# Kernel tuning notes

Measured on AMD Instinct MI355X. Metric: run time of the kernel, lower is better.

## Reference

```python
import jax, jax.numpy as jnp
import numpy as np

LEVEL = 3  # J
B3_TAPS = (1.0 / 16, 1.0 / 4, 3.0 / 8, 1.0 / 4, 1.0 / 16)  # h1, fixed non-trainable


def _b3_conv2d(x, d):
    """Separable 5-tap B3-spline conv with dilation d and reflect padding.

    Equivalent to torch Conv2d(1,1,5,dilation=d,padding=2*d,padding_mode='reflect')
    with weight = outer(h1, h1): the dense 5x5 kernel is separable.
    x: (B, H, W) -> (B, H, W)
    """
    w = [jnp.asarray(t, x.dtype) for t in B3_TAPS]
    pad = 2 * d  # effective half-width of dilated 5-tap kernel
    H, W = x.shape[1], x.shape[2]
    # conv along H
    xp = jnp.pad(x, ((0, 0), (pad, pad), (0, 0)), mode='reflect')
    x = sum(w[k] * xp[:, k * d:k * d + H, :] for k in range(5))
    # conv along W
    xp = jnp.pad(x, ((0, 0), (0, 0), (pad, pad)), mode='reflect')
    x = sum(w[k] * xp[:, :, k * d:k * d + W] for k in range(5))
    return x


def setup_inputs() -> dict:
    key = jax.random.key(0)
    x = jax.random.normal(key, (8, 1024, 1024), dtype=jnp.float32)
    return {"x": x}


def reference(x) -> jnp.ndarray:
    # c_j = h_j * c_{j-1};  w_j = c_{j-1} - c_j;  return [w_1..w_J, c_J] stacked on axis 1
    outs = []
    c = x
    for j in range(LEVEL):
        c_next = _b3_conv2d(c, 2 ** j)
        outs.append(c - c_next)
        c = c_next
    outs.append(c)
    return jnp.stack(outs, axis=1)  # (B, J+1, H, W)
```

## Files before the change

### kernel.cpp

```cpp
#include <hip/hip_runtime.h>

#define DEVINL __device__ __forceinline__


constexpr int W_IMG = 1024;
constexpr int H_IMG = 1024;
constexpr int TX = 32;
constexpr int TY = 32;
constexpr int HALO = 16;
constexpr int SW = 68;
constexpr int GXT = W_IMG / TX;
constexpr int GYT = H_IMG / TY;
constexpr int SHA = 60;
constexpr int SHB = 56;

constexpr float TP0 = 1.0f / 16.0f;
constexpr float TP1 = 1.0f / 4.0f;
constexpr float TP2 = 3.0f / 8.0f;

typedef float f32x4 __attribute__((ext_vector_type(4)));

template <int CTRL>
DEVINL float dppf(float x) {
    return __int_as_float(__builtin_amdgcn_update_dpp(
        0, __float_as_int(x), CTRL, 0xF, 0xF, true));
}

DEVINL int reflx(int g) {
    g = g < 0 ? -g : g;
    return g >= W_IMG ? 2 * W_IMG - 2 - g : g;
}

DEVINL void nt_store4(float* p, float a, float b, float c, float d) {
    f32x4 t;
    t.x = a; t.y = b; t.z = c; t.w = d;
    __builtin_nontemporal_store(t, (f32x4*)p);
}

DEVINL float4 ld4(const float* p) { return *(const float4*)p; }

DEVINL float4 vert(const float4& a0, const float4& a1, const float4& a2,
                   const float4& a3, const float4& a4) {
    float4 v;
    v.x = TP0 * (a0.x + a4.x) + TP1 * (a1.x + a3.x) + TP2 * a2.x;
    v.y = TP0 * (a0.y + a4.y) + TP1 * (a1.y + a3.y) + TP2 * a2.y;
    v.z = TP0 * (a0.z + a4.z) + TP1 * (a1.z + a3.z) + TP2 * a2.z;
    v.w = TP0 * (a0.w + a4.w) + TP1 * (a1.w + a3.w) + TP2 * a2.w;
    return v;
}

template <int D>
DEVINL float4 horiz(const float4& v) {
    float4 u;
    if constexpr (D == 1) {
        const float am2 = dppf<0x111>(v.z);
        const float am1 = dppf<0x111>(v.w);
        const float ap1 = dppf<0x101>(v.x);
        const float ap2 = dppf<0x101>(v.y);
        u.x = TP0 * (am2 + v.z) + TP1 * (am1 + v.y) + TP2 * v.x;
        u.y = TP0 * (am1 + v.w) + TP1 * (v.x + v.z) + TP2 * v.y;
        u.z = TP0 * (v.x + ap1) + TP1 * (v.y + v.w) + TP2 * v.z;
        u.w = TP0 * (v.y + ap2) + TP1 * (v.z + ap1) + TP2 * v.w;
    } else if constexpr (D == 2) {
        u.x = TP0 * (dppf<0x111>(v.x) + dppf<0x101>(v.x)) +
              TP1 * (dppf<0x111>(v.z) + v.z) + TP2 * v.x;
        u.y = TP0 * (dppf<0x111>(v.y) + dppf<0x101>(v.y)) +
              TP1 * (dppf<0x111>(v.w) + v.w) + TP2 * v.y;
        u.z = TP0 * (dppf<0x111>(v.z) + dppf<0x101>(v.z)) +
              TP1 * (v.x + dppf<0x101>(v.x)) + TP2 * v.z;
        u.w = TP0 * (dppf<0x111>(v.w) + dppf<0x101>(v.w)) +
              TP1 * (v.y + dppf<0x101>(v.y)) + TP2 * v.w;
    } else {
        u.x = TP0 * (dppf<0x112>(v.x) + dppf<0x102>(v.x)) +
              TP1 * (dppf<0x111>(v.x) + dppf<0x101>(v.x)) + TP2 * v.x;
        u.y = TP0 * (dppf<0x112>(v.y) + dppf<0x102>(v.y)) +
              TP1 * (dppf<0x111>(v.y) + dppf<0x101>(v.y)) + TP2 * v.y;
        u.z = TP0 * (dppf<0x112>(v.z) + dppf<0x102>(v.z)) +
              TP1 * (dppf<0x111>(v.z) + dppf<0x101>(v.z)) + TP2 * v.z;
        u.w = TP0 * (dppf<0x112>(v.w) + dppf<0x102>(v.w)) +
              TP1 * (dppf<0x111>(v.w) + dppf<0x101>(v.w)) + TP2 * v.w;
    }
    return u;
}

template <int D, int R0, int R1, int SOFF, int DOFF, int LVL, bool LAST>
DEVINL void do_level(const float* src, float* dst, float* obase, bool pok,
                     int ty, int c4) {
    constexpr size_t PL = (size_t)H_IMG * W_IMG;
    constexpr int KMAX = (R1 - R0 + 15) / 16;
#pragma unroll 2
    for (int k = 0; k < KMAX; ++k) {
        const int r = R0 + ty + 16 * k;
        if (r < R1) {
            const float* b = &src[(r - SOFF) * SW + c4];
            const float4 a0 = ld4(b - 2 * D * SW);
            const float4 a1 = ld4(b - D * SW);
            const float4 a2 = ld4(b);
            const float4 a3 = ld4(b + D * SW);
            const float4 a4 = ld4(b + 2 * D * SW);
            const float4 v = vert(a0, a1, a2, a3, a4);
            const float4 u = horiz<D>(v);
            const int ly = r - HALO;
            if (pok && (unsigned)ly < (unsigned)TY) {
                float* pw = obase + (size_t)LVL * PL + ((size_t)ly << 10);
                nt_store4(pw, a2.x - u.x, a2.y - u.y, a2.z - u.z, a2.w - u.w);
                if constexpr (LAST) {
                    float* pc = obase + (size_t)3 * PL + ((size_t)ly << 10);
                    nt_store4(pc, u.x, u.y, u.z, u.w);
                }
            }
            if constexpr (!LAST) *(float4*)&dst[(r - DOFF) * SW + c4] = u;
        }
    }
}

__global__ __launch_bounds__(256, 4) void uwt3(const float* __restrict__ x,
                                               float* __restrict__ out) {
    __shared__ __align__(16) float A[SHA * SW];
    __shared__ __align__(16) float B[SHB * SW];

    const int tid = threadIdx.x;
    const int p = tid & 15;
    const int ty = tid >> 4;
    int bid = blockIdx.x;
    const int bx = bid & 31;   bid >>= 5;
    const int by = bid & 31;
    const int b = bid >> 5;
    const int oy0 = by * TY;
    const int gx0 = bx * TX;
    const float* xb = x + (size_t)b * (H_IMG * W_IMG);
    const int c4 = p * 4;
    const bool edge = (bx == 0) || (bx == GXT - 1);
    const bool pok = (p >= 4) && (p < 12);
    float* obase = out + ((size_t)(b * 4) * H_IMG + oy0) * W_IMG +
                   (gx0 + c4 - HALO);

#pragma unroll 2
    for (int k = 0; k < 4; ++k) {
        const int sr = 2 + ty + 16 * k;
        if (sr < 62) {
            int gy = oy0 - HALO + sr;
            gy = gy < 0 ? -gy : gy;
            if (gy >= H_IMG) gy = 2 * H_IMG - 2 - gy;
            const float* row = xb + (size_t)gy * W_IMG;
            const int gx = gx0 - HALO + c4;
            float4 v;
            if (!edge) {
                v = *(const float4*)(row + gx);
            } else {
                v.x = row[reflx(gx)];
                v.y = row[reflx(gx + 1)];
                v.z = row[reflx(gx + 2)];
                v.w = row[reflx(gx + 3)];
            }
            *(float4*)&A[(sr - 2) * SW + c4] = v;
        }
    }
    __syncthreads();

    do_level<1, 4, 60, 2, 4, 0, false>(A, B, obase, pok, ty, c4);
    __syncthreads();
    do_level<2, 8, 56, 4, 8, 1, false>(B, A, obase, pok, ty, c4);
    __syncthreads();
    do_level<4, 16, 48, 8, 0, 2, true>(A, B, obase, pok, ty, c4);
}

extern "C" void kernel_launch(void* const* d_in, const int* in_sizes, int n_in,
                              void* d_out, int out_size, void* d_ws,
                              size_t ws_size, hipStream_t stream) {
    const float* x = (const float*)d_in[0];
    float* out = (float*)d_out;
    const int nb = in_sizes[0] / (H_IMG * W_IMG);
    dim3 grid(nb * GYT * GXT);
    uwt3<<<grid, 256, 0, stream>>>(x, out);
}
```

Before: 184.5 us.

## Widen column tile to 96 outputs with 8 columns per thread

Each thread now handles 8 columns instead of 4, so a block covers 128 columns of shared-memory tile (96 useful outputs plus 16-column halos) instead of 64 (32 useful). This cuts the redundant halo loads and compute from 2x overhead to about 1.33x, and the DPP neighbour exchange is restructured for the 8-wide lanes. The last column tile handles the ragged edge (11 tiles, fewer valid lanes). Shared memory per block roughly doubles and the occupancy hint drops to 2 blocks per CU, which may reduce latency hiding.

```diff
diff --git a/kernel.cpp b/kernel.cpp
--- a/kernel.cpp
+++ b/kernel.cpp
@@ -5,12 +5,12 @@
 
 constexpr int W_IMG = 1024;
 constexpr int H_IMG = 1024;
-constexpr int TX = 32;
+constexpr int TXO = 96;
 constexpr int TY = 32;
 constexpr int HALO = 16;
-constexpr int SW = 68;
-constexpr int GXT = W_IMG / TX;
-constexpr int GYT = H_IMG / TY;
+constexpr int SW = 132;
+constexpr int GXT = 11;
+constexpr int GYT = 32;
 constexpr int SHA = 60;
 constexpr int SHB = 56;
 
@@ -50,71 +50,106 @@
 }
 
 template <int D>
-DEVINL float4 horiz(const float4& v) {
-    float4 u;
+DEVINL void horiz8(const float4& vlo, const float4& vhi, float4& ulo,
+                   float4& uhi) {
     if constexpr (D == 1) {
-        const float am2 = dppf<0x111>(v.z);
-        const float am1 = dppf<0x111>(v.w);
-        const float ap1 = dppf<0x101>(v.x);
-        const float ap2 = dppf<0x101>(v.y);
-        u.x = TP0 * (am2 + v.z) + TP1 * (am1 + v.y) + TP2 * v.x;
-        u.y = TP0 * (am1 + v.w) + TP1 * (v.x + v.z) + TP2 * v.y;
-        u.z = TP0 * (v.x + ap1) + TP1 * (v.y + v.w) + TP2 * v.z;
-        u.w = TP0 * (v.y + ap2) + TP1 * (v.z + ap1) + TP2 * v.w;
+        const float pHz = dppf<0x111>(vhi.z);
+        const float pHw = dppf<0x111>(vhi.w);
+        const float nLx = dppf<0x101>(vlo.x);
+        const float nLy = dppf<0x101>(vlo.y);
+        ulo.x = TP0 * (pHz + vlo.z) + TP1 * (pHw + vlo.y) + TP2 * vlo.x;
+        ulo.y = TP0 * (pHw + vlo.w) + TP1 * (vlo.x + vlo.z) + TP2 * vlo.y;
+        ulo.z = TP0 * (vlo.x + vhi.x) + TP1 * (vlo.y + vlo.w) + TP2 * vlo.z;
+        ulo.w = TP0 * (vlo.y + vhi.y) + TP1 * (vlo.z + vhi.x) + TP2 * vlo.w;
+        uhi.x = TP0 * (vlo.z + vhi.z) + TP1 * (vlo.w + vhi.y) + TP2 * vhi.x;
+        uhi.y = TP0 * (vlo.w + vhi.w) + TP1 * (vhi.x + vhi.z) + TP2 * vhi.y;
+        uhi.z = TP0 * (vhi.x + nLx) + TP1 * (vhi.y + vhi.w) + TP2 * vhi.z;
+        uhi.w = TP0 * (vhi.y + nLy) + TP1 * (vhi.z + nLx) + TP2 * vhi.w;
     } else if constexpr (D == 2) {
-        u.x = TP0 * (dppf<0x111>(v.x) + dppf<0x101>(v.x)) +
-              TP1 * (dppf<0x111>(v.z) + v.z) + TP2 * v.x;
-        u.y = TP0 * (dppf<0x111>(v.y) + dppf<0x101>(v.y)) +
-              TP1 * (dppf<0x111>(v.w) + v.w) + TP2 * v.y;
-        u.z = TP0 * (dppf<0x111>(v.z) + dppf<0x101>(v.z)) +
-              TP1 * (v.x + dppf<0x101>(v.x)) + TP2 * v.z;
-        u.w = TP0 * (dppf<0x111>(v.w) + dppf<0x101>(v.w)) +
-              TP1 * (v.y + dppf<0x101>(v.y)) + TP2 * v.w;
+        const float pHx = dppf<0x111>(vhi.x);
+        const float pHy = dppf<0x111>(vhi.y);
+        const float pHz = dppf<0x111>(vhi.z);
+        const float pHw = dppf<0x111>(vhi.w);
+        const float nLx = dppf<0x101>(vlo.x);
+        const float nLy = dppf<0x101>(vlo.y);
+        const float nLz = dppf<0x101>(vlo.z);
+        const float nLw = dppf<0x101>(vlo.w);
+        ulo.x = TP0 * (pHx + vhi.x) + TP1 * (pHz + vlo.z) + TP2 * vlo.x;
+        ulo.y = TP0 * (pHy + vhi.y) + TP1 * (pHw + vlo.w) + TP2 * vlo.y;
+        ulo.z = TP0 * (pHz + vhi.z) + TP1 * (vlo.x + vhi.x) + TP2 * vlo.z;
+        ulo.w = TP0 * (pHw + vhi.w) + TP1 * (vlo.y + vhi.y) + TP2 * vlo.w;
+        uhi.x = TP0 * (vlo.x + nLx) + TP1 * (vlo.z + vhi.z) + TP2 * vhi.x;
+        uhi.y = TP0 * (vlo.y + nLy) + TP1 * (vlo.w + vhi.w) + TP2 * vhi.y;
+        uhi.z = TP0 * (vlo.z + nLz) + TP1 * (vhi.x + nLx) + TP2 * vhi.z;
+        uhi.w = TP0 * (vlo.w + nLw) + TP1 * (vhi.y + nLy) + TP2 * vhi.w;
     } else {
-        u.x = TP0 * (dppf<0x112>(v.x) + dppf<0x102>(v.x)) +
-              TP1 * (dppf<0x111>(v.x) + dppf<0x101>(v.x)) + TP2 * v.x;
-        u.y = TP0 * (dppf<0x112>(v.y) + dppf<0x102>(v.y)) +
-              TP1 * (dppf<0x111>(v.y) + dppf<0x101>(v.y)) + TP2 * v.y;
-        u.z = TP0 * (dppf<0x112>(v.z) + dppf<0x102>(v.z)) +
-              TP1 * (dppf<0x111>(v.z) + dppf<0x101>(v.z)) + TP2 * v.z;
-        u.w = TP0 * (dppf<0x112>(v.w) + dppf<0x102>(v.w)) +
-              TP1 * (dppf<0x111>(v.w) + dppf<0x101>(v.w)) + TP2 * v.w;
+        float4 pL, pH, nL, nH;
+        pL.x = dppf<0x111>(vlo.x); pL.y = dppf<0x111>(vlo.y);
+        pL.z = dppf<0x111>(vlo.z); pL.w = dppf<0x111>(vlo.w);
+        pH.x = dppf<0x111>(vhi.x); pH.y = dppf<0x111>(vhi.y);
+        pH.z = dppf<0x111>(vhi.z); pH.w = dppf<0x111>(vhi.w);
+        nL.x = dppf<0x101>(vlo.x); nL.y = dppf<0x101>(vlo.y);
+        nL.z = dppf<0x101>(vlo.z); nL.w = dppf<0x101>(vlo.w);
+        nH.x = dppf<0x101>(vhi.x); nH.y = dppf<0x101>(vhi.y);
+        nH.z = dppf<0x101>(vhi.z); nH.w = dppf<0x101>(vhi.w);
+        ulo.x = TP0 * (pL.x + nL.x) + TP1 * (pH.x + vhi.x) + TP2 * vlo.x;
+        ulo.y = TP0 * (pL.y + nL.y) + TP1 * (pH.y + vhi.y) + TP2 * vlo.y;
+        ulo.z = TP0 * (pL.z + nL.z) + TP1 * (pH.z + vhi.z) + TP2 * vlo.z;
+        ulo.w = TP0 * (pL.w + nL.w) + TP1 * (pH.w + vhi.w) + TP2 * vlo.w;
+        uhi.x = TP0 * (pH.x + nH.x) + TP1 * (vlo.x + nL.x) + TP2 * vhi.x;
+        uhi.y = TP0 * (pH.y + nH.y) + TP1 * (vlo.y + nL.y) + TP2 * vhi.y;
+        uhi.z = TP0 * (pH.z + nH.z) + TP1 * (vlo.z + nL.z) + TP2 * vhi.z;
+        uhi.w = TP0 * (pH.w + nH.w) + TP1 * (vlo.w + nL.w) + TP2 * vhi.w;
     }
-    return u;
-}
-
-template <int D, int R0, int R1, int SOFF, int DOFF, int LVL, bool LAST>
+}
+
+template <int D, int R0, int R1, int SOFF, int DOFF, int LVL, bool LAST,
+          bool GUARD>
 DEVINL void do_level(const float* src, float* dst, float* obase, bool pok,
-                     int ty, int c4) {
+                     int ty, int c8) {
     constexpr size_t PL = (size_t)H_IMG * W_IMG;
     constexpr int KMAX = (R1 - R0 + 15) / 16;
 #pragma unroll 2
     for (int k = 0; k < KMAX; ++k) {
         const int r = R0 + ty + 16 * k;
-        if (r < R1) {
-            const float* b = &src[(r - SOFF) * SW + c4];
-            const float4 a0 = ld4(b - 2 * D * SW);
-            const float4 a1 = ld4(b - D * SW);
-            const float4 a2 = ld4(b);
-            const float4 a3 = ld4(b + D * SW);
-            const float4 a4 = ld4(b + 2 * D * SW);
-            const float4 v = vert(a0, a1, a2, a3, a4);
-            const float4 u = horiz<D>(v);
+        if (!GUARD || r < R1) {
+            const float* bp = &src[(r - SOFF) * SW + c8];
+            const float4 l0 = ld4(bp - 2 * D * SW);
+            const float4 h0 = ld4(bp - 2 * D * SW + 4);
+            const float4 l1 = ld4(bp - D * SW);
+            const float4 h1 = ld4(bp - D * SW + 4);
+            const float4 l2 = ld4(bp);
+            const float4 h2 = ld4(bp + 4);
+            const float4 l3 = ld4(bp + D * SW);
+            const float4 h3 = ld4(bp + D * SW + 4);
+            const float4 l4 = ld4(bp + 2 * D * SW);
+            const float4 h4 = ld4(bp + 2 * D * SW + 4);
+            const float4 vlo = vert(l0, l1, l2, l3, l4);
+            const float4 vhi = vert(h0, h1, h2, h3, h4);
+            float4 ulo, uhi;
+            horiz8<D>(vlo, vhi, ulo, uhi);
             const int ly = r - HALO;
             if (pok && (unsigned)ly < (unsigned)TY) {
                 float* pw = obase + (size_t)LVL * PL + ((size_t)ly << 10);
-                nt_store4(pw, a2.x - u.x, a2.y - u.y, a2.z - u.z, a2.w - u.w);
+                nt_store4(pw, l2.x - ulo.x, l2.y - ulo.y, l2.z - ulo.z,
+                          l2.w - ulo.w);
+                nt_store4(pw + 4, h2.x - uhi.x, h2.y - uhi.y, h2.z - uhi.z,
+                          h2.w - uhi.w);
                 if constexpr (LAST) {
                     float* pc = obase + (size_t)3 * PL + ((size_t)ly << 10);
-                    nt_store4(pc, u.x, u.y, u.z, u.w);
+                    nt_store4(pc, ulo.x, ulo.y, ulo.z, ulo.w);
+                    nt_store4(pc + 4, uhi.x, uhi.y, uhi.z, uhi.w);
                 }
             }
-            if constexpr (!LAST) *(float4*)&dst[(r - DOFF) * SW + c4] = u;
+            if constexpr (!LAST) {
+                *(float4*)&dst[(r - DOFF) * SW + c8] = ulo;
+                *(float4*)&dst[(r - DOFF) * SW + c8 + 4] = uhi;
+            }
         }
     }
 }
 
-__global__ __launch_bounds__(256, 4) void uwt3(const float* __restrict__ x,
+__global__ __launch_bounds__(256, 2) void uwt3(const float* __restrict__ x,
                                                float* __restrict__ out) {
     __shared__ __align__(16) float A[SHA * SW];
     __shared__ __align__(16) float B[SHB * SW];
@@ -122,18 +157,20 @@
     const int tid = threadIdx.x;
     const int p = tid & 15;
     const int ty = tid >> 4;
-    int bid = blockIdx.x;
-    const int bx = bid & 31;   bid >>= 5;
-    const int by = bid & 31;
-    const int b = bid >> 5;
+    const int bid = blockIdx.x;
+    const int bx = bid % GXT;
+    const int rest = bid / GXT;
+    const int by = rest & 31;
+    const int b = rest >> 5;
     const int oy0 = by * TY;
-    const int gx0 = bx * TX;
+    const int gx0 = bx * TXO;
     const float* xb = x + (size_t)b * (H_IMG * W_IMG);
-    const int c4 = p * 4;
+    const int c8 = p * 8;
     const bool edge = (bx == 0) || (bx == GXT - 1);
-    const bool pok = (p >= 4) && (p < 12);
+    const int pmax = (bx == GXT - 1) ? 10 : 14;
+    const bool pok = (p >= 2) && (p < pmax);
     float* obase = out + ((size_t)(b * 4) * H_IMG + oy0) * W_IMG +
-                   (gx0 + c4 - HALO);
+                   (gx0 - HALO + c8);
 
 #pragma unroll 2
     for (int k = 0; k < 4; ++k) {
@@ -143,26 +180,32 @@
             gy = gy < 0 ? -gy : gy;
             if (gy >= H_IMG) gy = 2 * H_IMG - 2 - gy;
             const float* row = xb + (size_t)gy * W_IMG;
-            const int gx = gx0 - HALO + c4;
-            float4 v;
+            const int gx = gx0 - HALO + c8;
+            float4 vlo, vhi;
             if (!edge) {
-                v = *(const float4*)(row + gx);
+                vlo = *(const float4*)(row + gx);
+                vhi = *(const float4*)(row + gx + 4);
             } else {
-                v.x = row[reflx(gx)];
-                v.y = row[reflx(gx + 1)];
-                v.z = row[reflx(gx + 2)];
-                v.w = row[reflx(gx + 3)];
+                vlo.x = row[reflx(gx)];
+                vlo.y = row[reflx(gx + 1)];
+                vlo.z = row[reflx(gx + 2)];
+                vlo.w = row[reflx(gx + 3)];
+                vhi.x = row[reflx(gx + 4)];
+                vhi.y = row[reflx(gx + 5)];
+                vhi.z = row[reflx(gx + 6)];
+                vhi.w = row[reflx(gx + 7)];
             }
-            *(float4*)&A[(sr - 2) * SW + c4] = v;
+            *(float4*)&A[(sr - 2) * SW + c8] = vlo;
+            *(float4*)&A[(sr - 2) * SW + c8 + 4] = vhi;
         }
     }
     __syncthreads();
 
-    do_level<1, 4, 60, 2, 4, 0, false>(A, B, obase, pok, ty, c4);
+    do_level<1, 4, 60, 2, 4, 0, false, true>(A, B, obase, pok, ty, c8);
     __syncthreads();
-    do_level<2, 8, 56, 4, 8, 1, false>(B, A, obase, pok, ty, c4);
+    do_level<2, 8, 56, 4, 8, 1, false, false>(B, A, obase, pok, ty, c8);
     __syncthreads();
-    do_level<4, 16, 48, 8, 0, 2, true>(A, B, obase, pok, ty, c4);
+    do_level<4, 16, 48, 8, 0, 2, true, false>(A, B, obase, pok, ty, c8);
 }
 
 extern "C" void kernel_launch(void* const* d_in, const int* in_sizes, int n_in,
```

After: 190.8 us. 3.4% more time.
